# Kernel tuning notes

Measured on AMD Instinct MI355X. Metric: run time of the kernel, lower is better.

## Reference

```python
import jax, jax.numpy as jnp
import numpy as np

EPS = 1e-5  # torch group_norm default
GROUPS = 32


def _nin(t, W, b):
    # torch Nin: einsum('bchw,co->bowh') transposes spatial dims, then adds bias
    return jnp.einsum('bchw,co->bowh', t, W) + b


def setup_inputs() -> dict:
    key = jax.random.key(0)
    ks = jax.random.split(key, 9)
    B, C, N = 16, 512, 32
    x = jax.random.normal(ks[0], (B, C, N, N), jnp.float32)
    sc = 0.02
    Wq = jax.random.normal(ks[1], (C, C), jnp.float32) * sc
    Wk = jax.random.normal(ks[2], (C, C), jnp.float32) * sc
    Wv = jax.random.normal(ks[3], (C, C), jnp.float32) * sc
    Wn = jax.random.normal(ks[4], (C, C), jnp.float32) * sc
    bq = jnp.zeros((1, C, 1, 1), jnp.float32)
    bk = jnp.zeros((1, C, 1, 1), jnp.float32)
    bv = jnp.zeros((1, C, 1, 1), jnp.float32)
    bn = jnp.zeros((1, C, 1, 1), jnp.float32)
    return {"x": x, "Wq": Wq, "bq": bq, "Wk": Wk, "bk": bk,
            "Wv": Wv, "bv": bv, "Wn": Wn, "bn": bn}


def reference(x, Wq, bq, Wk, bk, Wv, bv, Wn, bn):
    B, C, H, W = x.shape
    # GroupNorm(32) with no affine params
    xg = x.reshape(B, GROUPS, -1)
    mu = xg.mean(-1, keepdims=True)
    var = xg.var(-1, keepdims=True)
    h = ((xg - mu) / jnp.sqrt(var + EPS)).reshape(B, C, H, W)
    # Nin projections -> spatially transposed (B, C, W, H)
    q = _nin(h, Wq, bq)
    k = _nin(h, Wk, bk)
    v = _nin(h, Wv, bv)
    # scores s[b,w1,w2,h1,h2] = sum_c q[b,c,w1,h1] k[b,c,w2,h2] * C^-0.5
    s = jnp.einsum('bcwh,bcWH->bwWhH', q, k) * (C ** -0.5)
    # softmax over flat (h1,h2) blocks exactly as the torch reshape does
    s = jax.nn.softmax(s.reshape(B, H, W, H * W), axis=-1).reshape(B, H, W, H, W)
    # torch.einsum('bHWHW, bcWH -> bcWH', w, v) takes the DIAGONAL over the
    # repeated H and W labels: diag[b,i,j] = s[b,i,j,i,j], then elementwise
    # scales v: out[b,c,w,h] = diag[b,h,w] * v[b,c,w,h]
    i = jnp.arange(H)
    j = jnp.arange(W)
    diag = s[:, i[:, None], j[None, :], i[:, None], j[None, :]]  # (B,H,W)
    h2 = v * jnp.swapaxes(diag, 1, 2)[:, None]  # (B,C,W,H)
    out = _nin(h2, Wn, bn)  # transposes back -> (B,C,H,W)
    return x + out
```

## Files before the change

### kernel.cpp

```cpp
#include <hip/hip_runtime.h>
#include <hip/hip_bf16.h>

typedef __attribute__((ext_vector_type(8))) short short8;
typedef __attribute__((ext_vector_type(4))) float floatx4;

#define MFMA16(a, b, c) __builtin_amdgcn_mfma_f32_16x16x32_bf16((a), (b), (c), 0, 0, 0)

__device__ __forceinline__ short f2bf(float f) {
    union { float f; unsigned u; } x; x.f = f;
    unsigned r = (x.u + 0x7fffu + ((x.u >> 16) & 1u)) >> 16;
    return (short)r;
}
__device__ __forceinline__ float bf2f(short s) {
    union { float f; unsigned u; } x; x.u = ((unsigned)(unsigned short)s) << 16;
    return x.f;
}

__device__ __forceinline__ void gl2lds16(const short* g, short* l) {
    void* gv = const_cast<short*>(g);
    __builtin_amdgcn_global_load_lds((__attribute__((address_space(1))) void*)gv,
                                     (__attribute__((address_space(3))) void*)l,
                                     16, 0, 0);
}

__global__ void prep_w(const float* __restrict__ Wq, const float* __restrict__ Wk,
                       const float* __restrict__ Wv, const float* __restrict__ Wn,
                       short* __restrict__ wqb, short* __restrict__ wkb,
                       short* __restrict__ Wtv, short* __restrict__ Wn_t) {
    __shared__ float t[32][33];
    int z = blockIdx.z;
    int o0 = blockIdx.x * 32, c0 = blockIdx.y * 32;
    int lx = threadIdx.x, ly = threadIdx.y;
    if (z < 2) {
        const float* src = z ? Wk : Wq;
        short* dst = z ? wkb : wqb;
        for (int i = ly; i < 32; i += 8)
            dst[(size_t)(c0 + i) * 512 + o0 + lx] = f2bf(src[(size_t)(c0 + i) * 512 + o0 + lx]);
    } else {
        const float* src = (z == 2) ? Wv : Wn;
        short* dst = (z == 2) ? (Wtv + (size_t)512 * 512) : Wn_t;
        for (int i = ly; i < 32; i += 8) t[i][lx] = src[(size_t)(c0 + i) * 512 + o0 + lx];
        __syncthreads();
        for (int i = ly; i < 32; i += 8) dst[(size_t)(o0 + i) * 512 + c0 + lx] = f2bf(t[lx][i]);
    }
}

__global__ void prep_vec(const float* __restrict__ Wq, const float* __restrict__ Wk,
                         const float* __restrict__ bq, const float* __restrict__ bk,
                         float* __restrict__ wu, float* __restrict__ wv2,
                         float* __restrict__ cstp) {
    int c = blockIdx.x, ln = threadIdx.x;
    float su = 0.f, sv = 0.f;
    for (int o = ln; o < 512; o += 64) {
        su += Wq[(size_t)c * 512 + o] * bk[o];
        sv += Wk[(size_t)c * 512 + o] * bq[o];
    }
#pragma unroll
    for (int off = 32; off > 0; off >>= 1) {
        su += __shfl_down(su, off, 64);
        sv += __shfl_down(sv, off, 64);
    }
    if (ln == 0) { wu[c] = su; wv2[c] = sv; }
    if (c == 0) {
        float sc = 0.f;
        for (int o = ln; o < 512; o += 64) sc += bq[o] * bk[o];
#pragma unroll
        for (int off = 32; off > 0; off >>= 1) sc += __shfl_down(sc, off, 64);
        if (ln == 0) cstp[0] = sc;
    }
}

__global__ __launch_bounds__(256) void g_gemm(const short* __restrict__ A,
                                              const short* __restrict__ B,
                                              short* __restrict__ Out) {
    const int tid = threadIdx.x;
    const int wv = tid >> 6, ln = tid & 63;
    const int m0 = blockIdx.x * 128, n0 = blockIdx.y * 128;
    __shared__ __attribute__((aligned(16))) short As[128 * 32];
    __shared__ __attribute__((aligned(16))) short Bs[128 * 32];
    floatx4 acc[4][4] = {};
    const int wm = (wv >> 1) * 64, wn = (wv & 1) * 64;
    const int fr = ln & 15, fq = ln >> 4;
    for (int kk = 0; kk < 512; kk += 32) {
        __syncthreads();
#pragma unroll
        for (int j = 0; j < 2; ++j) {
            int s = (wv * 2 + j) * 64 + ln;
            int r = s >> 2;
            int q = (s & 3) ^ ((r >> 1) & 3);
            gl2lds16(A + (size_t)(m0 + r) * 512 + kk + q * 8, As + (size_t)(wv * 2 + j) * 512);
            gl2lds16(B + (size_t)(n0 + r) * 512 + kk + q * 8, Bs + (size_t)(wv * 2 + j) * 512);
        }
        __syncthreads();
        short8 af[4], bfr[4];
#pragma unroll
        for (int t = 0; t < 4; ++t) {
            int ra = wm + t * 16 + fr;
            af[t]  = *(const short8*)(As + ra * 32 + ((fq ^ ((ra >> 1) & 3)) * 8));
            int rb = wn + t * 16 + fr;
            bfr[t] = *(const short8*)(Bs + rb * 32 + ((fq ^ ((rb >> 1) & 3)) * 8));
        }
#pragma unroll
        for (int mt = 0; mt < 4; ++mt)
#pragma unroll
            for (int nt = 0; nt < 4; ++nt)
                acc[mt][nt] = MFMA16(af[mt], bfr[nt], acc[mt][nt]);
    }
#pragma unroll
    for (int mt = 0; mt < 4; ++mt)
#pragma unroll
        for (int nt = 0; nt < 4; ++nt) {
            int n = n0 + wn + nt * 16 + fr;
#pragma unroll
            for (int r = 0; r < 4; ++r) {
                int m = m0 + wm + mt * 16 + fq * 4 + r;
                Out[(size_t)m * 512 + n] = f2bf(acc[mt][nt][r]);
            }
        }
}

__global__ __launch_bounds__(256) void groupnorm_k(const float* __restrict__ x,
                                                   short* __restrict__ hnt) {
    int b = blockIdx.x >> 5, g = blockIdx.x & 31;
    const float* xg = x + ((size_t)b * 512 + g * 16) * 1024;
    const float4* xg4 = (const float4*)xg;
    float s = 0.f, ss = 0.f;
    for (int i = threadIdx.x; i < 4096; i += 256) {
        float4 v = xg4[i];
        s  += v.x + v.y + v.z + v.w;
        ss += v.x * v.x + v.y * v.y + v.z * v.z + v.w * v.w;
    }
#pragma unroll
    for (int off = 32; off > 0; off >>= 1) {
        s  += __shfl_down(s,  off, 64);
        ss += __shfl_down(ss, off, 64);
    }
    __shared__ float red[8];
    int w = threadIdx.x >> 6;
    if ((threadIdx.x & 63) == 0) { red[w] = s; red[4 + w] = ss; }
    __syncthreads();
    float S  = red[0] + red[1] + red[2] + red[3];
    float SS = red[4] + red[5] + red[6] + red[7];
    float mean = S * (1.f / 16384.f);
    float var  = SS * (1.f / 16384.f) - mean * mean;
    float rstd = rsqrtf(var + 1e-5f);
    __shared__ __attribute__((aligned(16))) short tile[16 * 1026];
    for (int i = threadIdx.x; i < 4096; i += 256) {
        float4 v = xg4[i];
        int c = i >> 8, p = (i & 255) * 4;
        short* tp = tile + c * 1026 + p;
        tp[0] = f2bf((v.x - mean) * rstd);
        tp[1] = f2bf((v.y - mean) * rstd);
        tp[2] = f2bf((v.z - mean) * rstd);
        tp[3] = f2bf((v.w - mean) * rstd);
    }
    __syncthreads();
    for (int i = threadIdx.x; i < 2048; i += 256) {
        int p = i >> 1, half = i & 1;
        short8 v;
#pragma unroll
        for (int j = 0; j < 8; ++j) v[j] = tile[(half * 8 + j) * 1026 + p];
        *(short8*)(hnt + ((size_t)b * 1024 + p) * 512 + g * 16 + half * 8) = v;
    }
}

__global__ __launch_bounds__(256) void uv_gemv(const short* __restrict__ hnt,
                                               const float* __restrict__ wu,
                                               const float* __restrict__ wv2,
                                               float* __restrict__ u1p,
                                               float* __restrict__ v2p) {
    __shared__ float wus[512], wvs[512];
    for (int i = threadIdx.x; i < 512; i += 256) { wus[i] = wu[i]; wvs[i] = wv2[i]; }
    __syncthreads();
    int wv_ = threadIdx.x >> 6, ln = threadIdx.x & 63;
    int row = blockIdx.x * 4 + wv_;
    int b = row >> 10, p = row & 1023;
    short8 h = *(const short8*)(hnt + (size_t)row * 512 + ln * 8);
    float su = 0.f, sv = 0.f;
#pragma unroll
    for (int j = 0; j < 8; ++j) {
        float hv = bf2f(h[j]);
        su += hv * wus[ln * 8 + j];
        sv += hv * wvs[ln * 8 + j];
    }
#pragma unroll
    for (int off = 32; off > 0; off >>= 1) {
        su += __shfl_down(su, off, 64);
        sv += __shfl_down(sv, off, 64);
    }
    if (ln == 0) {
        int pp = ((p & 31) << 5) | (p >> 5);
        u1p[b * 1024 + pp] = su;
        v2p[b * 1024 + pp] = sv;
    }
}

__global__ __launch_bounds__(256, 2) void tv_gemm(const short* __restrict__ A,
                                                  const short* __restrict__ Wt,
                                                  const float* __restrict__ bv,
                                                  short* __restrict__ T,
                                                  short* __restrict__ Vb) {
    const int tid = threadIdx.x;
    const int wv = tid >> 6, ln = tid & 63;
    const int m0 = blockIdx.x * 256, n0 = blockIdx.y * 128;
    const size_t BS = 1024 * 512;
    const short* Ab = A + (size_t)blockIdx.z * BS;
    const int tsel = n0 >> 9;
    short* Ob = (tsel ? Vb : T) + (size_t)blockIdx.z * BS;

    __shared__ __attribute__((aligned(16))) short As[256 * 32];
    __shared__ __attribute__((aligned(16))) short Bs[128 * 32];

    floatx4 acc[8][4] = {};
    const int wm = (wv >> 1) * 128, wn = (wv & 1) * 64;
    const int fr = ln & 15, fq = ln >> 4;

    for (int kk = 0; kk < 512; kk += 32) {
        __syncthreads();
#pragma unroll
        for (int j = 0; j < 4; ++j) {
            int s = (wv * 4 + j) * 64 + ln;
            int r = s >> 2;
            int q = (s & 3) ^ ((r >> 1) & 3);
            gl2lds16(Ab + (size_t)(m0 + r) * 512 + kk + q * 8, As + (size_t)(wv * 4 + j) * 512);
        }
#pragma unroll
        for (int j = 0; j < 2; ++j) {
            int s = (wv * 2 + j) * 64 + ln;
            int r = s >> 2;
            int q = (s & 3) ^ ((r >> 1) & 3);
            gl2lds16(Wt + (size_t)(n0 + r) * 512 + kk + q * 8, Bs + (size_t)(wv * 2 + j) * 512);
        }
        __syncthreads();
        short8 af[8], bfr[4];
#pragma unroll
        for (int t = 0; t < 8; ++t) {
            int ra = wm + t * 16 + fr;
            af[t] = *(const short8*)(As + ra * 32 + ((fq ^ ((ra >> 1) & 3)) * 8));
        }
#pragma unroll
        for (int u = 0; u < 4; ++u) {
            int rb = wn + u * 16 + fr;
            bfr[u] = *(const short8*)(Bs + rb * 32 + ((fq ^ ((rb >> 1) & 3)) * 8));
        }
#pragma unroll
        for (int mt = 0; mt < 8; ++mt)
#pragma unroll
            for (int nt = 0; nt < 4; ++nt)
                acc[mt][nt] = MFMA16(af[mt], bfr[nt], acc[mt][nt]);
    }
#pragma unroll
    for (int mt = 0; mt < 8; ++mt)
#pragma unroll
        for (int nt = 0; nt < 4; ++nt) {
            int n = n0 + wn + nt * 16 + fr;
            float bvv = tsel ? bv[n - 512] : 0.0f;
            int nn = n & 511;
#pragma unroll
            for (int r = 0; r < 4; ++r) {
                int m = m0 + wm + mt * 16 + fq * 4 + r;
                Ob[(size_t)m * 512 + nn] = f2bf(acc[mt][nt][r] + bvv);
            }
        }
}

__global__ __launch_bounds__(256, 2) void attn_sm(const short* __restrict__ Tt,
                                                  const short* __restrict__ Hn,
                                                  const float* __restrict__ u1p,
                                                  const float* __restrict__ v2p,
                                                  const float* __restrict__ cstp,
                                                  float* __restrict__ Dm) {
    const int tid = threadIdx.x;
    const int wv = tid >> 6, ln = tid & 63;
    const int m0 = blockIdx.x * 128, n0 = blockIdx.y * 256, b = blockIdx.z;
    const short* Tb = Tt + (size_t)b * (1024 * 512);
    const short* Hb = Hn + (size_t)b * (1024 * 512);

    __shared__ __attribute__((aligned(16))) short As[128 * 32];
    __shared__ __attribute__((aligned(16))) short Bs[256 * 32];

    floatx4 acc[4][8] = {};
    const int wm = (wv >> 1) * 64, wn = (wv & 1) * 128;
    const int fr = ln & 15, fq = ln >> 4;

    size_t offA[2], offB[4];
#pragma unroll
    for (int j = 0; j < 2; ++j) {
        int s = (wv * 2 + j) * 64 + ln;
        int r = s >> 2;
        int q = (s & 3) ^ ((r >> 1) & 3);
        int m = m0 + r;
        int pm = ((m & 31) << 5) | (m >> 5);
        offA[j] = (size_t)pm * 512 + q * 8;
    }
#pragma unroll
    for (int j = 0; j < 4; ++j) {
        int s = (wv * 4 + j) * 64 + ln;
        int r = s >> 2;
        int q = (s & 3) ^ ((r >> 1) & 3);
        int m = n0 + r;
        int pm = ((m & 31) << 5) | (m >> 5);
        offB[j] = (size_t)pm * 512 + q * 8;
    }

    for (int kk = 0; kk < 512; kk += 32) {
        __syncthreads();
#pragma unroll
        for (int j = 0; j < 2; ++j)
            gl2lds16(Tb + offA[j] + kk, As + (size_t)(wv * 2 + j) * 512);
#pragma unroll
        for (int j = 0; j < 4; ++j)
            gl2lds16(Hb + offB[j] + kk, Bs + (size_t)(wv * 4 + j) * 512);
        __syncthreads();
        short8 af[4], bfr[8];
#pragma unroll
        for (int t = 0; t < 4; ++t) {
            int ra = wm + t * 16 + fr;
            af[t] = *(const short8*)(As + ra * 32 + ((fq ^ ((ra >> 1) & 3)) * 8));
        }
#pragma unroll
        for (int u = 0; u < 8; ++u) {
            int rb = wn + u * 16 + fr;
            bfr[u] = *(const short8*)(Bs + rb * 32 + ((fq ^ ((rb >> 1) & 3)) * 8));
        }
#pragma unroll
        for (int mt = 0; mt < 4; ++mt)
#pragma unroll
            for (int nt = 0; nt < 8; ++nt)
                acc[mt][nt] = MFMA16(af[mt], bfr[nt], acc[mt][nt]);
    }

    const float scale = 0.04419417382415922f;
    const float cst = cstp[0];
    const int wbase = (m0 + wm) >> 5;
    const int Wbase = (n0 + wn) >> 5;
#pragma unroll
    for (int si = 0; si < 2; ++si) {
#pragma unroll
        for (int sj = 0; sj < 4; ++sj) {
            int wg = wbase + si, Wg = Wbase + sj;
            float tv[16];
            float mx = -3.0e38f;
#pragma unroll
            for (int mi = 0; mi < 2; ++mi)
#pragma unroll
                for (int ni = 0; ni < 2; ++ni) {
                    float vc = v2p[b * 1024 + Wg * 32 + ni * 16 + fr];
#pragma unroll
                    for (int r = 0; r < 4; ++r) {
                        float uc = u1p[b * 1024 + wg * 32 + mi * 16 + fq * 4 + r];
                        float u = (acc[2 * si + mi][2 * sj + ni][r] + uc + vc + cst) * scale;
                        tv[(mi * 2 + ni) * 4 + r] = u;
                        mx = fmaxf(mx, u);
                    }
                }
#pragma unroll
            for (int off = 32; off > 0; off >>= 1) mx = fmaxf(mx, __shfl_xor(mx, off, 64));
            float se = 0.f;
#pragma unroll
            for (int i = 0; i < 16; ++i) se += __expf(tv[i] - mx);
#pragma unroll
            for (int off = 32; off > 0; off >>= 1) se += __shfl_xor(se, off, 64);
            if (fq == ((wg >> 2) & 3) && fr == (Wg & 15)) {
                int mi = wg >> 4, ni = Wg >> 4;
                float numer = tv[(mi * 2 + ni) * 4 + (wg & 3)];
                Dm[((size_t)b * 32 + wg) * 32 + Wg] = __expf(numer - mx) / se;
            }
        }
    }
}

__global__ __launch_bounds__(256) void out_gemm(const short* __restrict__ A,
                                                const short* __restrict__ Wt,
                                                const float* __restrict__ Dm,
                                                const float* __restrict__ bnb,
                                                const float* __restrict__ x,
                                                float* __restrict__ out) {
    const int tid = threadIdx.x;
    const int wv = tid >> 6, ln = tid & 63;
    const int m0 = blockIdx.x * 128, n0 = blockIdx.y * 128, b = blockIdx.z;
    const size_t BS = 1024 * 512;
    const short* Ab = A + (size_t)b * BS;

    __shared__ __attribute__((aligned(16))) short As[128 * 32];
    __shared__ __attribute__((aligned(16))) short Bs[128 * 32];

    floatx4 acc[4][4] = {};
    const int wm = (wv >> 1) * 64, wn = (wv & 1) * 64;
    const int fr = ln & 15, fq = ln >> 4;

    for (int kk = 0; kk < 512; kk += 32) {
        __syncthreads();
#pragma unroll
        for (int j = 0; j < 2; ++j) {
            int s = (wv * 2 + j) * 64 + ln;
            int r = s >> 2;
            int q = (s & 3) ^ ((r >> 1) & 3);
            gl2lds16(Ab + (size_t)(m0 + r) * 512 + kk + q * 8, As + (size_t)(wv * 2 + j) * 512);
            gl2lds16(Wt + (size_t)(n0 + r) * 512 + kk + q * 8, Bs + (size_t)(wv * 2 + j) * 512);
        }
        __syncthreads();
        short8 af[4], bfr[4];
#pragma unroll
        for (int t = 0; t < 4; ++t) {
            int ra = wm + t * 16 + fr;
            af[t]  = *(const short8*)(As + ra * 32 + ((fq ^ ((ra >> 1) & 3)) * 8));
            int rb = wn + t * 16 + fr;
            bfr[t] = *(const short8*)(Bs + rb * 32 + ((fq ^ ((rb >> 1) & 3)) * 8));
        }
#pragma unroll
        for (int mt = 0; mt < 4; ++mt)
#pragma unroll
            for (int nt = 0; nt < 4; ++nt)
                acc[mt][nt] = MFMA16(af[mt], bfr[nt], acc[mt][nt]);
    }
#pragma unroll
    for (int mt = 0; mt < 4; ++mt) {
        int mbase = m0 + wm + mt * 16 + fq * 4;
        float4 d4 = *(const float4*)(Dm + (size_t)b * 1024 + mbase);
#pragma unroll
        for (int nt = 0; nt < 4; ++nt) {
            int n = n0 + wn + nt * 16 + fr;
            float bvv = bnb[n];
            size_t base = ((size_t)b * 512 + n) * 1024 + mbase;
            float4 x4 = *(const float4*)(x + base);
            float4 o;
            o.x = x4.x + d4.x * acc[mt][nt][0] + bvv;
            o.y = x4.y + d4.y * acc[mt][nt][1] + bvv;
            o.z = x4.z + d4.z * acc[mt][nt][2] + bvv;
            o.w = x4.w + d4.w * acc[mt][nt][3] + bvv;
            *(float4*)(out + base) = o;
        }
    }
}

extern "C" void kernel_launch(void* const* d_in, const int* in_sizes, int n_in,
                              void* d_out, int out_size, void* d_ws, size_t ws_size,
                              hipStream_t stream) {
    const float* x  = (const float*)d_in[0];
    const float* Wq = (const float*)d_in[1];
    const float* bq = (const float*)d_in[2];
    const float* Wk = (const float*)d_in[3];
    const float* bk = (const float*)d_in[4];
    const float* Wv = (const float*)d_in[5];
    const float* bv = (const float*)d_in[6];
    const float* Wn = (const float*)d_in[7];
    const float* bn = (const float*)d_in[8];
    float* out = (float*)d_out;
    char* ws = (char*)d_ws;

    const size_t WSZ = (size_t)512 * 512 * 2;
    const size_t TSZ = (size_t)16 * 1024 * 512 * 2;
    short* wqb  = (short*)(ws);
    short* wkb  = (short*)(ws + WSZ);
    short* Wtv  = (short*)(ws + 2 * WSZ);
    short* Wn_t = (short*)(ws + 4 * WSZ);
    float* wu   = (float*)(ws + 5 * WSZ);
    float* wv2  = (float*)(ws + 5 * WSZ + 2048);
    float* cstp = (float*)(ws + 5 * WSZ + 4096);
    char*  base = ws + 5 * WSZ + 8192;
    short* hnt = (short*)(base);
    short* T   = (short*)(base + TSZ);
    short* Vb  = (short*)(base + 2 * TSZ);
    float* u1p = (float*)(base + 3 * TSZ);
    float* v2p = (float*)(base + 3 * TSZ + 65536);
    float* Dm  = (float*)(base + 3 * TSZ + 131072);

    prep_w<<<dim3(16, 16, 4), dim3(32, 8), 0, stream>>>(Wq, Wk, Wv, Wn, wqb, wkb, Wtv, Wn_t);
    g_gemm<<<dim3(4, 4, 1), 256, 0, stream>>>(wkb, wqb, Wtv);
    prep_vec<<<512, 64, 0, stream>>>(Wq, Wk, bq, bk, wu, wv2, cstp);
    groupnorm_k<<<512, 256, 0, stream>>>(x, hnt);
    uv_gemv<<<4096, 256, 0, stream>>>(hnt, wu, wv2, u1p, v2p);
    tv_gemm<<<dim3(4, 8, 16), 256, 0, stream>>>(hnt, Wtv, bv, T, Vb);
    attn_sm<<<dim3(8, 4, 16), 256, 0, stream>>>(T, hnt, u1p, v2p, cstp, Dm);
    out_gemm<<<dim3(8, 4, 16), 256, 0, stream>>>(Vb, Wn_t, Dm, bn, x, out);
}
```

Before: 222.9 us.

## Fuse prep and gemv kernels, pre-permute layouts, remap blocks per XCD

```diff
diff --git a/kernel.cpp b/kernel.cpp
--- a/kernel.cpp
+++ b/kernel.cpp
@@ -25,48 +25,39 @@
 
 __global__ void prep_w(const float* __restrict__ Wq, const float* __restrict__ Wk,
                        const float* __restrict__ Wv, const float* __restrict__ Wn,
+                       const float* __restrict__ bq, const float* __restrict__ bk,
                        short* __restrict__ wqb, short* __restrict__ wkb,
-                       short* __restrict__ Wtv, short* __restrict__ Wn_t) {
+                       short* __restrict__ Wtv, short* __restrict__ Wn_t,
+                       float* __restrict__ wu, float* __restrict__ wv2,
+                       float* __restrict__ cstp) {
     __shared__ float t[32][33];
     int z = blockIdx.z;
     int o0 = blockIdx.x * 32, c0 = blockIdx.y * 32;
     int lx = threadIdx.x, ly = threadIdx.y;
     if (z < 2) {
-        const float* src = z ? Wk : Wq;
-        short* dst = z ? wkb : wqb;
-        for (int i = ly; i < 32; i += 8)
-            dst[(size_t)(c0 + i) * 512 + o0 + lx] = f2bf(src[(size_t)(c0 + i) * 512 + o0 + lx]);
+        const float* src  = z ? Wk : Wq;
+        const float* bvec = z ? bq : bk;
+        short* dst  = z ? wkb : wqb;
+        float* ddst = z ? wv2 : wu;
+        float bvl = bvec[o0 + lx];
+        for (int i = ly; i < 32; i += 8) {
+            float v = src[(size_t)(c0 + i) * 512 + o0 + lx];
+            dst[(size_t)(c0 + i) * 512 + o0 + lx] = f2bf(v);
+            float d = v * bvl;
+#pragma unroll
+            for (int off = 16; off > 0; off >>= 1) d += __shfl_down(d, off, 32);
+            if (lx == 0) atomicAdd(&ddst[c0 + i], d);
+        }
+        if (z == 0 && blockIdx.x == 0 && blockIdx.y == 0) {
+            int t0 = ly * 32 + lx;
+            atomicAdd(cstp, bq[t0] * bk[t0] + bq[t0 + 256] * bk[t0 + 256]);
+        }
     } else {
         const float* src = (z == 2) ? Wv : Wn;
         short* dst = (z == 2) ? (Wtv + (size_t)512 * 512) : Wn_t;
         for (int i = ly; i < 32; i += 8) t[i][lx] = src[(size_t)(c0 + i) * 512 + o0 + lx];
         __syncthreads();
         for (int i = ly; i < 32; i += 8) dst[(size_t)(o0 + i) * 512 + c0 + lx] = f2bf(t[lx][i]);
-    }
-}
-
-__global__ void prep_vec(const float* __restrict__ Wq, const float* __restrict__ Wk,
-                         const float* __restrict__ bq, const float* __restrict__ bk,
-                         float* __restrict__ wu, float* __restrict__ wv2,
-                         float* __restrict__ cstp) {
-    int c = blockIdx.x, ln = threadIdx.x;
-    float su = 0.f, sv = 0.f;
-    for (int o = ln; o < 512; o += 64) {
-        su += Wq[(size_t)c * 512 + o] * bk[o];
-        sv += Wk[(size_t)c * 512 + o] * bq[o];
-    }
-#pragma unroll
-    for (int off = 32; off > 0; off >>= 1) {
-        su += __shfl_down(su, off, 64);
-        sv += __shfl_down(sv, off, 64);
-    }
-    if (ln == 0) { wu[c] = su; wv2[c] = sv; }
-    if (c == 0) {
-        float sc = 0.f;
-        for (int o = ln; o < 512; o += 64) sc += bq[o] * bk[o];
-#pragma unroll
-        for (int off = 32; off > 0; off >>= 1) sc += __shfl_down(sc, off, 64);
-        if (ln == 0) cstp[0] = sc;
     }
 }
 
@@ -120,7 +111,12 @@
 }
 
 __global__ __launch_bounds__(256) void groupnorm_k(const float* __restrict__ x,
-                                                   short* __restrict__ hnt) {
+                                                   const float* __restrict__ wu,
+                                                   const float* __restrict__ wv2,
+                                                   short* __restrict__ hnt,
+                                                   short* __restrict__ Hp,
+                                                   float* __restrict__ u1p,
+                                                   float* __restrict__ v2p) {
     int b = blockIdx.x >> 5, g = blockIdx.x & 31;
     const float* xg = x + ((size_t)b * 512 + g * 16) * 1024;
     const float4* xg4 = (const float4*)xg;
@@ -136,8 +132,11 @@
         ss += __shfl_down(ss, off, 64);
     }
     __shared__ float red[8];
+    __shared__ float wus[16], wvs[16];
     int w = threadIdx.x >> 6;
     if ((threadIdx.x & 63) == 0) { red[w] = s; red[4 + w] = ss; }
+    if (threadIdx.x < 16) wus[threadIdx.x] = wu[g * 16 + threadIdx.x];
+    else if (threadIdx.x < 32) wvs[threadIdx.x - 16] = wv2[g * 16 + threadIdx.x - 16];
     __syncthreads();
     float S  = red[0] + red[1] + red[2] + red[3];
     float SS = red[4] + red[5] + red[6] + red[7];
@@ -157,100 +156,78 @@
     __syncthreads();
     for (int i = threadIdx.x; i < 2048; i += 256) {
         int p = i >> 1, half = i & 1;
+        int pp = ((p & 31) << 5) | (p >> 5);
         short8 v;
 #pragma unroll
         for (int j = 0; j < 8; ++j) v[j] = tile[(half * 8 + j) * 1026 + p];
-        *(short8*)(hnt + ((size_t)b * 1024 + p) * 512 + g * 16 + half * 8) = v;
-    }
-}
-
-__global__ __launch_bounds__(256) void uv_gemv(const short* __restrict__ hnt,
-                                               const float* __restrict__ wu,
-                                               const float* __restrict__ wv2,
-                                               float* __restrict__ u1p,
-                                               float* __restrict__ v2p) {
-    __shared__ float wus[512], wvs[512];
-    for (int i = threadIdx.x; i < 512; i += 256) { wus[i] = wu[i]; wvs[i] = wv2[i]; }
-    __syncthreads();
-    int wv_ = threadIdx.x >> 6, ln = threadIdx.x & 63;
-    int row = blockIdx.x * 4 + wv_;
-    int b = row >> 10, p = row & 1023;
-    short8 h = *(const short8*)(hnt + (size_t)row * 512 + ln * 8);
-    float su = 0.f, sv = 0.f;
-#pragma unroll
-    for (int j = 0; j < 8; ++j) {
-        float hv = bf2f(h[j]);
-        su += hv * wus[ln * 8 + j];
-        sv += hv * wvs[ln * 8 + j];
-    }
-#pragma unroll
-    for (int off = 32; off > 0; off >>= 1) {
-        su += __shfl_down(su, off, 64);
-        sv += __shfl_down(sv, off, 64);
-    }
-    if (ln == 0) {
+        *(short8*)(hnt + ((size_t)b * 1024 + p)  * 512 + g * 16 + half * 8) = v;
+        *(short8*)(Hp  + ((size_t)b * 1024 + pp) * 512 + g * 16 + half * 8) = v;
+    }
+    for (int p = threadIdx.x; p < 1024; p += 256) {
+        float su = 0.f, sv = 0.f;
+#pragma unroll
+        for (int c = 0; c < 16; ++c) {
+            float hv = bf2f(tile[c * 1026 + p]);
+            su += hv * wus[c];
+            sv += hv * wvs[c];
+        }
         int pp = ((p & 31) << 5) | (p >> 5);
-        u1p[b * 1024 + pp] = su;
-        v2p[b * 1024 + pp] = sv;
-    }
-}
-
-__global__ __launch_bounds__(256, 2) void tv_gemm(const short* __restrict__ A,
-                                                  const short* __restrict__ Wt,
-                                                  const float* __restrict__ bv,
-                                                  short* __restrict__ T,
-                                                  short* __restrict__ Vb) {
+        atomicAdd(&u1p[b * 1024 + pp], su);
+        atomicAdd(&v2p[b * 1024 + pp], sv);
+    }
+}
+
+__global__ __launch_bounds__(256) void tv_gemm(const short* __restrict__ A,
+                                               const short* __restrict__ Wt,
+                                               const float* __restrict__ bv,
+                                               short* __restrict__ T,
+                                               short* __restrict__ Vb) {
     const int tid = threadIdx.x;
     const int wv = tid >> 6, ln = tid & 63;
-    const int m0 = blockIdx.x * 256, n0 = blockIdx.y * 128;
+    int sid = blockIdx.x + 8 * (blockIdx.y + 8 * blockIdx.z);
+    int xcd = sid & 7, chunk = sid >> 3;
+    int bz = xcd * 2 + (chunk >> 6);
+    int inner = chunk & 63;
+    const int m0 = (inner & 7) * 128, n0 = (inner >> 3) * 128;
     const size_t BS = 1024 * 512;
-    const short* Ab = A + (size_t)blockIdx.z * BS;
+    const short* Ab = A + (size_t)bz * BS;
     const int tsel = n0 >> 9;
-    short* Ob = (tsel ? Vb : T) + (size_t)blockIdx.z * BS;
-
-    __shared__ __attribute__((aligned(16))) short As[256 * 32];
+    short* Ob = (tsel ? Vb : T) + (size_t)bz * BS;
+
+    __shared__ __attribute__((aligned(16))) short As[128 * 32];
     __shared__ __attribute__((aligned(16))) short Bs[128 * 32];
 
-    floatx4 acc[8][4] = {};
-    const int wm = (wv >> 1) * 128, wn = (wv & 1) * 64;
+    floatx4 acc[4][4] = {};
+    const int wm = (wv >> 1) * 64, wn = (wv & 1) * 64;
     const int fr = ln & 15, fq = ln >> 4;
 
     for (int kk = 0; kk < 512; kk += 32) {
         __syncthreads();
-#pragma unroll
-        for (int j = 0; j < 4; ++j) {
-            int s = (wv * 4 + j) * 64 + ln;
-            int r = s >> 2;
-            int q = (s & 3) ^ ((r >> 1) & 3);
-            gl2lds16(Ab + (size_t)(m0 + r) * 512 + kk + q * 8, As + (size_t)(wv * 4 + j) * 512);
-        }
 #pragma unroll
         for (int j = 0; j < 2; ++j) {
             int s = (wv * 2 + j) * 64 + ln;
             int r = s >> 2;
             int q = (s & 3) ^ ((r >> 1) & 3);
+            gl2lds16(Ab + (size_t)(m0 + r) * 512 + kk + q * 8, As + (size_t)(wv * 2 + j) * 512);
             gl2lds16(Wt + (size_t)(n0 + r) * 512 + kk + q * 8, Bs + (size_t)(wv * 2 + j) * 512);
         }
         __syncthreads();
-        short8 af[8], bfr[4];
-#pragma unroll
-        for (int t = 0; t < 8; ++t) {
+        short8 af[4], bfr[4];
+#pragma unroll
+        for (int t = 0; t < 4; ++t) {
             int ra = wm + t * 16 + fr;
-            af[t] = *(const short8*)(As + ra * 32 + ((fq ^ ((ra >> 1) & 3)) * 8));
-        }
-#pragma unroll
-        for (int u = 0; u < 4; ++u) {
-            int rb = wn + u * 16 + fr;
-            bfr[u] = *(const short8*)(Bs + rb * 32 + ((fq ^ ((rb >> 1) & 3)) * 8));
-        }
-#pragma unroll
-        for (int mt = 0; mt < 8; ++mt)
+            af[t]  = *(const short8*)(As + ra * 32 + ((fq ^ ((ra >> 1) & 3)) * 8));
+            int rb = wn + t * 16 + fr;
+            bfr[t] = *(const short8*)(Bs + rb * 32 + ((fq ^ ((rb >> 1) & 3)) * 8));
+        }
+#pragma unroll
+        for (int mt = 0; mt < 4; ++mt)
 #pragma unroll
             for (int nt = 0; nt < 4; ++nt)
                 acc[mt][nt] = MFMA16(af[mt], bfr[nt], acc[mt][nt]);
     }
 #pragma unroll
-    for (int mt = 0; mt < 8; ++mt)
+    for (int mt = 0; mt < 4; ++mt)
 #pragma unroll
         for (int nt = 0; nt < 4; ++nt) {
             int n = n0 + wn + nt * 16 + fr;
@@ -259,22 +236,27 @@
 #pragma unroll
             for (int r = 0; r < 4; ++r) {
                 int m = m0 + wm + mt * 16 + fq * 4 + r;
-                Ob[(size_t)m * 512 + nn] = f2bf(acc[mt][nt][r] + bvv);
+                int mrow = tsel ? m : (((m & 31) << 5) | (m >> 5));
+                Ob[(size_t)mrow * 512 + nn] = f2bf(acc[mt][nt][r] + bvv);
             }
         }
 }
 
 __global__ __launch_bounds__(256, 2) void attn_sm(const short* __restrict__ Tt,
-                                                  const short* __restrict__ Hn,
+                                                  const short* __restrict__ Hp,
                                                   const float* __restrict__ u1p,
                                                   const float* __restrict__ v2p,
                                                   const float* __restrict__ cstp,
                                                   float* __restrict__ Dm) {
     const int tid = threadIdx.x;
     const int wv = tid >> 6, ln = tid & 63;
-    const int m0 = blockIdx.x * 128, n0 = blockIdx.y * 256, b = blockIdx.z;
+    int sid = blockIdx.x + 8 * (blockIdx.y + 4 * blockIdx.z);
+    int xcd = sid & 7, chunk = sid >> 3;
+    int b = xcd * 2 + (chunk >> 5);
+    int inner = chunk & 31;
+    const int m0 = (inner & 7) * 128, n0 = (inner >> 3) * 256;
     const short* Tb = Tt + (size_t)b * (1024 * 512);
-    const short* Hb = Hn + (size_t)b * (1024 * 512);
+    const short* Hb = Hp + (size_t)b * (1024 * 512);
 
     __shared__ __attribute__((aligned(16))) short As[128 * 32];
     __shared__ __attribute__((aligned(16))) short Bs[256 * 32];
@@ -283,34 +265,22 @@
     const int wm = (wv >> 1) * 64, wn = (wv & 1) * 128;
     const int fr = ln & 15, fq = ln >> 4;
 
-    size_t offA[2], offB[4];
-#pragma unroll
-    for (int j = 0; j < 2; ++j) {
-        int s = (wv * 2 + j) * 64 + ln;
-        int r = s >> 2;
-        int q = (s & 3) ^ ((r >> 1) & 3);
-        int m = m0 + r;
-        int pm = ((m & 31) << 5) | (m >> 5);
-        offA[j] = (size_t)pm * 512 + q * 8;
-    }
-#pragma unroll
-    for (int j = 0; j < 4; ++j) {
-        int s = (wv * 4 + j) * 64 + ln;
-        int r = s >> 2;
-        int q = (s & 3) ^ ((r >> 1) & 3);
-        int m = n0 + r;
-        int pm = ((m & 31) << 5) | (m >> 5);
-        offB[j] = (size_t)pm * 512 + q * 8;
-    }
-
     for (int kk = 0; kk < 512; kk += 32) {
         __syncthreads();
 #pragma unroll
-        for (int j = 0; j < 2; ++j)
-            gl2lds16(Tb + offA[j] + kk, As + (size_t)(wv * 2 + j) * 512);
-#pragma unroll
-        for (int j = 0; j < 4; ++j)
-            gl2lds16(Hb + offB[j] + kk, Bs + (size_t)(wv * 4 + j) * 512);
+        for (int j = 0; j < 2; ++j) {
+            int s = (wv * 2 + j) * 64 + ln;
+            int r = s >> 2;
+            int q = (s & 3) ^ ((r >> 1) & 3);
+            gl2lds16(Tb + (size_t)(m0 + r) * 512 + kk + q * 8, As + (size_t)(wv * 2 + j) * 512);
+        }
+#pragma unroll
+        for (int j = 0; j < 4; ++j) {
+            int s = (wv * 4 + j) * 64 + ln;
+            int r = s >> 2;
+            int q = (s & 3) ^ ((r >> 1) & 3);
+            gl2lds16(Hb + (size_t)(n0 + r) * 512 + kk + q * 8, Bs + (size_t)(wv * 4 + j) * 512);
+        }
         __syncthreads();
         short8 af[4], bfr[8];
 #pragma unroll
@@ -378,7 +348,11 @@
                                                 float* __restrict__ out) {
     const int tid = threadIdx.x;
     const int wv = tid >> 6, ln = tid & 63;
-    const int m0 = blockIdx.x * 128, n0 = blockIdx.y * 128, b = blockIdx.z;
+    int sid = blockIdx.x + 8 * (blockIdx.y + 4 * blockIdx.z);
+    int xcd = sid & 7, chunk = sid >> 3;
+    int b = xcd * 2 + (chunk >> 5);
+    int inner = chunk & 31;
+    const int m0 = (inner & 7) * 128, n0 = (inner >> 3) * 128;
     const size_t BS = 1024 * 512;
     const short* Ab = A + (size_t)b * BS;
 
@@ -451,27 +425,29 @@
 
     const size_t WSZ = (size_t)512 * 512 * 2;
     const size_t TSZ = (size_t)16 * 1024 * 512 * 2;
-    short* wqb  = (short*)(ws);
-    short* wkb  = (short*)(ws + WSZ);
-    short* Wtv  = (short*)(ws + 2 * WSZ);
-    short* Wn_t = (short*)(ws + 4 * WSZ);
-    float* wu   = (float*)(ws + 5 * WSZ);
-    float* wv2  = (float*)(ws + 5 * WSZ + 2048);
-    float* cstp = (float*)(ws + 5 * WSZ + 4096);
-    char*  base = ws + 5 * WSZ + 8192;
+    short* Wtv  = (short*)(ws);
+    short* Wn_t = (short*)(ws + 2 * WSZ);
+    float* wu   = (float*)(ws + 3 * WSZ);
+    float* wv2  = wu + 512;
+    float* cstp = wv2 + 512;
+    float* u1p  = cstp + 16;
+    float* v2p  = u1p + 16384;
+    const size_t ZB = (512 + 512 + 16 + 16384 + 16384) * sizeof(float);
+    char* base = ws + 3 * WSZ + 139264;
     short* hnt = (short*)(base);
-    short* T   = (short*)(base + TSZ);
-    short* Vb  = (short*)(base + 2 * TSZ);
-    float* u1p = (float*)(base + 3 * TSZ);
-    float* v2p = (float*)(base + 3 * TSZ + 65536);
-    float* Dm  = (float*)(base + 3 * TSZ + 131072);
-
-    prep_w<<<dim3(16, 16, 4), dim3(32, 8), 0, stream>>>(Wq, Wk, Wv, Wn, wqb, wkb, Wtv, Wn_t);
+    short* Hp  = (short*)(base + TSZ);
+    short* T   = (short*)(base + 2 * TSZ);
+    short* Vb  = (short*)(base + 3 * TSZ);
+    float* Dm  = (float*)(base + 4 * TSZ);
+    short* wqb = Hp;
+    short* wkb = Hp + 512 * 512;
+
+    hipMemsetAsync(wu, 0, ZB, stream);
+    prep_w<<<dim3(16, 16, 4), dim3(32, 8), 0, stream>>>(
+        Wq, Wk, Wv, Wn, bq, bk, wqb, wkb, Wtv, Wn_t, wu, wv2, cstp);
     g_gemm<<<dim3(4, 4, 1), 256, 0, stream>>>(wkb, wqb, Wtv);
-    prep_vec<<<512, 64, 0, stream>>>(Wq, Wk, bq, bk, wu, wv2, cstp);
-    groupnorm_k<<<512, 256, 0, stream>>>(x, hnt);
-    uv_gemv<<<4096, 256, 0, stream>>>(hnt, wu, wv2, u1p, v2p);
-    tv_gemm<<<dim3(4, 8, 16), 256, 0, stream>>>(hnt, Wtv, bv, T, Vb);
-    attn_sm<<<dim3(8, 4, 16), 256, 0, stream>>>(T, hnt, u1p, v2p, cstp, Dm);
+    groupnorm_k<<<512, 256, 0, stream>>>(x, wu, wv2, hnt, Hp, u1p, v2p);
+    tv_gemm<<<dim3(8, 8, 16), 256, 0, stream>>>(hnt, Wtv, bv, T, Vb);
+    attn_sm<<<dim3(8, 4, 16), 256, 0, stream>>>(T, Hp, u1p, v2p, cstp, Dm);
     out_gemm<<<dim3(8, 4, 16), 256, 0, stream>>>(Vb, Wn_t, Dm, bn, x, out);
 }
```

Measured after the change: 244.5 us. +9.7%, slower.

## Remap GEMM blocks per XCD, shrink tv_gemm tiles, fold prep_vec into prep_w

Applied to the files above, without the earlier changes.

```diff
diff --git a/kernel.cpp b/kernel.cpp
--- a/kernel.cpp
+++ b/kernel.cpp
@@ -25,48 +25,55 @@
 
 __global__ void prep_w(const float* __restrict__ Wq, const float* __restrict__ Wk,
                        const float* __restrict__ Wv, const float* __restrict__ Wn,
+                       const float* __restrict__ bq, const float* __restrict__ bk,
                        short* __restrict__ wqb, short* __restrict__ wkb,
-                       short* __restrict__ Wtv, short* __restrict__ Wn_t) {
+                       short* __restrict__ Wtv, short* __restrict__ Wn_t,
+                       float* __restrict__ wu, float* __restrict__ wv2,
+                       float* __restrict__ cstp) {
     __shared__ float t[32][33];
+    __shared__ float cred[4];
     int z = blockIdx.z;
     int o0 = blockIdx.x * 32, c0 = blockIdx.y * 32;
     int lx = threadIdx.x, ly = threadIdx.y;
+    int tid = ly * 32 + lx;
     if (z < 2) {
         const float* src = z ? Wk : Wq;
         short* dst = z ? wkb : wqb;
         for (int i = ly; i < 32; i += 8)
             dst[(size_t)(c0 + i) * 512 + o0 + lx] = f2bf(src[(size_t)(c0 + i) * 512 + o0 + lx]);
-    } else {
+    } else if (z < 4) {
         const float* src = (z == 2) ? Wv : Wn;
         short* dst = (z == 2) ? (Wtv + (size_t)512 * 512) : Wn_t;
         for (int i = ly; i < 32; i += 8) t[i][lx] = src[(size_t)(c0 + i) * 512 + o0 + lx];
         __syncthreads();
         for (int i = ly; i < 32; i += 8) dst[(size_t)(o0 + i) * 512 + c0 + lx] = f2bf(t[lx][i]);
-    }
-}
-
-__global__ void prep_vec(const float* __restrict__ Wq, const float* __restrict__ Wk,
-                         const float* __restrict__ bq, const float* __restrict__ bk,
-                         float* __restrict__ wu, float* __restrict__ wv2,
-                         float* __restrict__ cstp) {
-    int c = blockIdx.x, ln = threadIdx.x;
-    float su = 0.f, sv = 0.f;
-    for (int o = ln; o < 512; o += 64) {
-        su += Wq[(size_t)c * 512 + o] * bk[o];
-        sv += Wk[(size_t)c * 512 + o] * bq[o];
-    }
-#pragma unroll
-    for (int off = 32; off > 0; off >>= 1) {
-        su += __shfl_down(su, off, 64);
-        sv += __shfl_down(sv, off, 64);
-    }
-    if (ln == 0) { wu[c] = su; wv2[c] = sv; }
-    if (c == 0) {
+    } else {
+        if (blockIdx.y != 0) return;
+        int cb = blockIdx.x * 32;
+        int cl = tid >> 3, part = tid & 7;
+        float su = 0.f, sv = 0.f;
+        const float* wqr = Wq + (size_t)(cb + cl) * 512;
+        const float* wkr = Wk + (size_t)(cb + cl) * 512;
+        for (int o = part * 64; o < part * 64 + 64; ++o) {
+            su += wqr[o] * bk[o];
+            sv += wkr[o] * bq[o];
+        }
+        t[cl][part] = su;
+        t[cl][part + 8] = sv;
         float sc = 0.f;
-        for (int o = ln; o < 512; o += 64) sc += bq[o] * bk[o];
+        if (blockIdx.x == 0) sc = bq[tid] * bk[tid] + bq[tid + 256] * bk[tid + 256];
 #pragma unroll
         for (int off = 32; off > 0; off >>= 1) sc += __shfl_down(sc, off, 64);
-        if (ln == 0) cstp[0] = sc;
+        if ((tid & 63) == 0) cred[tid >> 6] = sc;
+        __syncthreads();
+        if (part == 0) {
+            float a = 0.f, b2 = 0.f;
+#pragma unroll
+            for (int j = 0; j < 8; ++j) { a += t[cl][j]; b2 += t[cl][j + 8]; }
+            wu[cb + cl] = a;
+            wv2[cb + cl] = b2;
+        }
+        if (blockIdx.x == 0 && tid == 0) cstp[0] = cred[0] + cred[1] + cred[2] + cred[3];
     }
 }
 
@@ -195,62 +202,57 @@
     }
 }
 
-__global__ __launch_bounds__(256, 2) void tv_gemm(const short* __restrict__ A,
-                                                  const short* __restrict__ Wt,
-                                                  const float* __restrict__ bv,
-                                                  short* __restrict__ T,
-                                                  short* __restrict__ Vb) {
+__global__ __launch_bounds__(256) void tv_gemm(const short* __restrict__ A,
+                                               const short* __restrict__ Wt,
+                                               const float* __restrict__ bv,
+                                               short* __restrict__ T,
+                                               short* __restrict__ Vb) {
     const int tid = threadIdx.x;
     const int wv = tid >> 6, ln = tid & 63;
-    const int m0 = blockIdx.x * 256, n0 = blockIdx.y * 128;
+    int sid = blockIdx.x + 8 * (blockIdx.y + 8 * blockIdx.z);
+    int xcd = sid & 7, chunk = sid >> 3;
+    int bz = xcd * 2 + (chunk >> 6);
+    int inner = chunk & 63;
+    const int m0 = (inner & 7) * 128, n0 = (inner >> 3) * 128;
     const size_t BS = 1024 * 512;
-    const short* Ab = A + (size_t)blockIdx.z * BS;
+    const short* Ab = A + (size_t)bz * BS;
     const int tsel = n0 >> 9;
-    short* Ob = (tsel ? Vb : T) + (size_t)blockIdx.z * BS;
-
-    __shared__ __attribute__((aligned(16))) short As[256 * 32];
+    short* Ob = (tsel ? Vb : T) + (size_t)bz * BS;
+
+    __shared__ __attribute__((aligned(16))) short As[128 * 32];
     __shared__ __attribute__((aligned(16))) short Bs[128 * 32];
 
-    floatx4 acc[8][4] = {};
-    const int wm = (wv >> 1) * 128, wn = (wv & 1) * 64;
+    floatx4 acc[4][4] = {};
+    const int wm = (wv >> 1) * 64, wn = (wv & 1) * 64;
     const int fr = ln & 15, fq = ln >> 4;
 
     for (int kk = 0; kk < 512; kk += 32) {
         __syncthreads();
-#pragma unroll
-        for (int j = 0; j < 4; ++j) {
-            int s = (wv * 4 + j) * 64 + ln;
-            int r = s >> 2;
-            int q = (s & 3) ^ ((r >> 1) & 3);
-            gl2lds16(Ab + (size_t)(m0 + r) * 512 + kk + q * 8, As + (size_t)(wv * 4 + j) * 512);
-        }
 #pragma unroll
         for (int j = 0; j < 2; ++j) {
             int s = (wv * 2 + j) * 64 + ln;
             int r = s >> 2;
             int q = (s & 3) ^ ((r >> 1) & 3);
+            gl2lds16(Ab + (size_t)(m0 + r) * 512 + kk + q * 8, As + (size_t)(wv * 2 + j) * 512);
             gl2lds16(Wt + (size_t)(n0 + r) * 512 + kk + q * 8, Bs + (size_t)(wv * 2 + j) * 512);
         }
         __syncthreads();
-        short8 af[8], bfr[4];
-#pragma unroll
-        for (int t = 0; t < 8; ++t) {
+        short8 af[4], bfr[4];
+#pragma unroll
+        for (int t = 0; t < 4; ++t) {
             int ra = wm + t * 16 + fr;
-            af[t] = *(const short8*)(As + ra * 32 + ((fq ^ ((ra >> 1) & 3)) * 8));
-        }
-#pragma unroll
-        for (int u = 0; u < 4; ++u) {
-            int rb = wn + u * 16 + fr;
-            bfr[u] = *(const short8*)(Bs + rb * 32 + ((fq ^ ((rb >> 1) & 3)) * 8));
-        }
-#pragma unroll
-        for (int mt = 0; mt < 8; ++mt)
+            af[t]  = *(const short8*)(As + ra * 32 + ((fq ^ ((ra >> 1) & 3)) * 8));
+            int rb = wn + t * 16 + fr;
+            bfr[t] = *(const short8*)(Bs + rb * 32 + ((fq ^ ((rb >> 1) & 3)) * 8));
+        }
+#pragma unroll
+        for (int mt = 0; mt < 4; ++mt)
 #pragma unroll
             for (int nt = 0; nt < 4; ++nt)
                 acc[mt][nt] = MFMA16(af[mt], bfr[nt], acc[mt][nt]);
     }
 #pragma unroll
-    for (int mt = 0; mt < 8; ++mt)
+    for (int mt = 0; mt < 4; ++mt)
 #pragma unroll
         for (int nt = 0; nt < 4; ++nt) {
             int n = n0 + wn + nt * 16 + fr;
@@ -272,7 +274,11 @@
                                                   float* __restrict__ Dm) {
     const int tid = threadIdx.x;
     const int wv = tid >> 6, ln = tid & 63;
-    const int m0 = blockIdx.x * 128, n0 = blockIdx.y * 256, b = blockIdx.z;
+    int sid = blockIdx.x + 8 * (blockIdx.y + 4 * blockIdx.z);
+    int xcd = sid & 7, chunk = sid >> 3;
+    int b = xcd * 2 + (chunk >> 5);
+    int inner = chunk & 31;
+    const int m0 = (inner & 7) * 128, n0 = (inner >> 3) * 256;
     const short* Tb = Tt + (size_t)b * (1024 * 512);
     const short* Hb = Hn + (size_t)b * (1024 * 512);
 
@@ -378,7 +384,11 @@
                                                 float* __restrict__ out) {
     const int tid = threadIdx.x;
     const int wv = tid >> 6, ln = tid & 63;
-    const int m0 = blockIdx.x * 128, n0 = blockIdx.y * 128, b = blockIdx.z;
+    int sid = blockIdx.x + 8 * (blockIdx.y + 4 * blockIdx.z);
+    int xcd = sid & 7, chunk = sid >> 3;
+    int b = xcd * 2 + (chunk >> 5);
+    int inner = chunk & 31;
+    const int m0 = (inner & 7) * 128, n0 = (inner >> 3) * 128;
     const size_t BS = 1024 * 512;
     const short* Ab = A + (size_t)b * BS;
 
@@ -451,27 +461,27 @@
 
     const size_t WSZ = (size_t)512 * 512 * 2;
     const size_t TSZ = (size_t)16 * 1024 * 512 * 2;
-    short* wqb  = (short*)(ws);
-    short* wkb  = (short*)(ws + WSZ);
-    short* Wtv  = (short*)(ws + 2 * WSZ);
-    short* Wn_t = (short*)(ws + 4 * WSZ);
-    float* wu   = (float*)(ws + 5 * WSZ);
-    float* wv2  = (float*)(ws + 5 * WSZ + 2048);
-    float* cstp = (float*)(ws + 5 * WSZ + 4096);
-    char*  base = ws + 5 * WSZ + 8192;
+    short* Wtv  = (short*)(ws);
+    short* Wn_t = (short*)(ws + 2 * WSZ);
+    float* wu   = (float*)(ws + 3 * WSZ);
+    float* wv2  = wu + 512;
+    float* cstp = wv2 + 512;
+    float* u1p  = cstp + 16;
+    float* v2p  = u1p + 16384;
+    char* base = ws + 3 * WSZ + 139264;
     short* hnt = (short*)(base);
     short* T   = (short*)(base + TSZ);
     short* Vb  = (short*)(base + 2 * TSZ);
-    float* u1p = (float*)(base + 3 * TSZ);
-    float* v2p = (float*)(base + 3 * TSZ + 65536);
-    float* Dm  = (float*)(base + 3 * TSZ + 131072);
-
-    prep_w<<<dim3(16, 16, 4), dim3(32, 8), 0, stream>>>(Wq, Wk, Wv, Wn, wqb, wkb, Wtv, Wn_t);
+    float* Dm  = (float*)(base + 3 * TSZ);
+    short* wqb = T;
+    short* wkb = T + 512 * 512;
+
+    prep_w<<<dim3(16, 16, 5), dim3(32, 8), 0, stream>>>(
+        Wq, Wk, Wv, Wn, bq, bk, wqb, wkb, Wtv, Wn_t, wu, wv2, cstp);
     g_gemm<<<dim3(4, 4, 1), 256, 0, stream>>>(wkb, wqb, Wtv);
-    prep_vec<<<512, 64, 0, stream>>>(Wq, Wk, bq, bk, wu, wv2, cstp);
     groupnorm_k<<<512, 256, 0, stream>>>(x, hnt);
     uv_gemv<<<4096, 256, 0, stream>>>(hnt, wu, wv2, u1p, v2p);
-    tv_gemm<<<dim3(4, 8, 16), 256, 0, stream>>>(hnt, Wtv, bv, T, Vb);
+    tv_gemm<<<dim3(8, 8, 16), 256, 0, stream>>>(hnt, Wtv, bv, T, Vb);
     attn_sm<<<dim3(8, 4, 16), 256, 0, stream>>>(T, hnt, u1p, v2p, cstp, Dm);
     out_gemm<<<dim3(8, 4, 16), 256, 0, stream>>>(Vb, Wn_t, Dm, bn, x, out);
 }
```

New measurement: 219.5 us. About the same (-1.5%).
